# Performance work log

Measured on AMD Instinct MI355X. Metric: run time of the kernel, lower is better.

## Reference

```python
import jax, jax.numpy as jnp
import numpy as np

B, L, S, V = 1024, 512, 64, 160000
EMB = 16
E = 3 * EMB            # extended embedding dim = 48
G, M = 4, 3            # lsh_group_num, lsh_group_length
MAXC = 2 ** M          # 8 buckets per group
NH, KD = 8, 4          # MHA heads / key_dim
IN_DIM = 5 * EMB + 3 * E   # user(80) + item(48) + longterm(48) + shortterm(48) = 224
PAD_LT, PAD_ST = L // 4, S // 4
M_VALUES = jnp.array([1, 2, 4], dtype=jnp.float32)
LN_EPS = 1e-3  # keras LayerNormalization default


def setup_inputs() -> dict:
    key = jax.random.key(0)
    ks = list(jax.random.split(key, 40))
    d = {}
    for i, n in enumerate(['uid', 'utag1', 'utag2', 'utag3', 'utag4']):
        d[n] = jax.random.randint(ks[i], (B,), 1, V, dtype=jnp.int32)
    for i, n in enumerate(['label_goods_ids', 'label_shop_ids', 'label_cate_ids']):
        d[n] = jax.random.randint(ks[5 + i], (B,), 1, V, dtype=jnp.int32)
    for i, n in enumerate(['longterm_goods_ids', 'longterm_shop_ids', 'longterm_cate_ids']):
        ids = jax.random.randint(ks[8 + i], (B, L), 1, V, dtype=jnp.int32)
        d[n] = ids.at[:, L - PAD_LT:].set(0)  # left-aligned valid prefix, padded tail
    for i, n in enumerate(['shortterm_goods_ids', 'shortterm_shop_ids', 'shortterm_cate_ids']):
        ids = jax.random.randint(ks[11 + i], (B, S), 1, V, dtype=jnp.int32)
        d[n] = ids.at[:, S - PAD_ST:].set(0)
    def nrm(k, shape, s):
        return jax.random.normal(k, shape, jnp.float32) * s
    d['embed_table'] = nrm(ks[14], (V, EMB), 0.05)
    d['H'] = nrm(ks[15], (E, G, M), 1.0)  # non-trainable LSH projections
    d['wq'] = nrm(ks[16], (E, NH, KD), 0.1); d['bq'] = jnp.zeros((NH, KD))
    d['wk'] = nrm(ks[17], (E, NH, KD), 0.1); d['bk'] = jnp.zeros((NH, KD))
    d['wv'] = nrm(ks[18], (E, NH, KD), 0.1); d['bv'] = jnp.zeros((NH, KD))
    d['wo'] = nrm(ks[19], (NH, KD, E), 0.1); d['bo'] = jnp.zeros((E,))
    d['w1'] = nrm(ks[20], (IN_DIM, 200), 0.1); d['b1'] = jnp.zeros((200,))
    d['g1'] = jnp.ones((200,)); d['be1'] = jnp.zeros((200,))
    d['w2'] = nrm(ks[21], (200, 80), 0.1); d['b2'] = jnp.zeros((80,))
    d['g2'] = jnp.ones((80,)); d['be2'] = jnp.zeros((80,))
    d['w3'] = nrm(ks[22], (80, 1), 0.1); d['b3'] = jnp.zeros((1,))
    return d


def _stack_embed(table, feats):
    # feats: list of (B,) or (B,T) int arrays -> (B, T, n_feats*EMB)
    cols = [f[:, None] if f.ndim == 1 else f for f in feats]
    X = jnp.stack(cols, axis=2)              # (B, T, F)
    Xe = table[X]                            # (B, T, F, EMB)
    return Xe.reshape(Xe.shape[0], Xe.shape[1], -1)


def _layernorm(x, g, b):
    mu = x.mean(-1, keepdims=True)
    var = jnp.square(x - mu).mean(-1, keepdims=True)
    return g * (x - mu) / jnp.sqrt(var + LN_EPS) + b


def _lsh_codes(x, H):
    # x: (B, T, E) -> integer bucket codes (B, T, G)
    codes = jnp.sign(jnp.einsum('bte,egm->btgm', x, H))
    binary = (codes == 1).astype(jnp.float32)
    return jnp.tensordot(binary, M_VALUES, axes=[[-1], [0]]).astype(jnp.int32)


def _forward(uid, utag1, utag2, utag3, utag4,
             label_goods_ids, label_shop_ids, label_cate_ids,
             longterm_goods_ids, longterm_shop_ids, longterm_cate_ids,
             shortterm_goods_ids, shortterm_shop_ids, shortterm_cate_ids,
             embed_table, H, wq, bq, wk, bk, wv, bv, wo, bo,
             w1, b1, g1, be1, w2, b2, g2, be2, w3, b3):
    # --- embeddings ---
    Xu = _stack_embed(embed_table, [uid, utag1, utag2, utag3, utag4])        # (B,1,80)
    Xi = _stack_embed(embed_table, [label_goods_ids, label_shop_ids, label_cate_ids])  # (B,1,48)
    Xl = _stack_embed(embed_table, [longterm_goods_ids, longterm_shop_ids, longterm_cate_ids])   # (B,L,48)
    Xs = _stack_embed(embed_table, [shortterm_goods_ids, shortterm_shop_ids, shortterm_cate_ids])  # (B,S,48)

    longterm_pad = longterm_goods_ids == 0
    shortterm_pad = shortterm_goods_ids == 0

    # --- long-term interest: LSH scatter-mean over buckets then gather by item code ---
    series_int = _lsh_codes(Xl, H)                                   # (B,L,G)
    mXl = Xl * (~longterm_pad).astype(jnp.float32)[:, :, None]        # masked series embeddings
    oh = jax.nn.one_hot(series_int, MAXC, dtype=jnp.float32)          # (B,L,G,C)
    c_sum = jnp.einsum('blgc,ble->bgce', oh, mXl)                     # bucket sums (B,G,C,E)
    vc = oh.sum(axis=1)                                               # valid counts (B,G,C)
    safe = jnp.where(vc[..., None] > 0,
                     c_sum / jnp.maximum(vc[..., None], 1.0),
                     0.0)                                             # bucket means
    item_int = _lsh_codes(Xi, H)                                      # (B,1,G)
    item_oh = jax.nn.one_hot(item_int, MAXC, dtype=jnp.float32)       # (B,1,G,C)
    longterm_interest = jnp.einsum('bgce,bsgc->bsge', safe, item_oh).mean(axis=2)  # (B,1,E)

    # --- short-term interest: target attention (keras MultiHeadAttention) ---
    lengths = (~shortterm_pad).astype(jnp.int32).sum(axis=1)           # (B,)
    seq_mask = (jnp.arange(S)[None, :] < lengths[:, None]).astype(jnp.float32)  # (B,S)
    q = jnp.einsum('bqe,ehd->bqhd', Xi, wq) + bq
    k = jnp.einsum('bke,ehd->bkhd', Xs, wk) + bk
    v = jnp.einsum('bke,ehd->bkhd', Xs, wv) + bv
    scores = jnp.einsum('bqhd,bkhd->bhqk', q, k) / jnp.sqrt(jnp.float32(KD))
    scores = scores + (1.0 - seq_mask[:, None, None, :]) * (-1e9)
    attn = jax.nn.softmax(scores, axis=-1)
    ctx = jnp.einsum('bhqk,bkhd->bqhd', attn, v)
    shortterm_interest = jnp.einsum('bqhd,hde->bqe', ctx, wo) + bo      # (B,1,E)

    # --- final MLP: Dense->LN->ReLU x2, Dense->sigmoid ---
    feat = jnp.concatenate([Xu[:, 0], Xi[:, 0],
                            longterm_interest[:, 0], shortterm_interest[:, 0]], axis=-1)  # (B,224)
    h = jax.nn.relu(_layernorm(feat @ w1 + b1, g1, be1))
    h = jax.nn.relu(_layernorm(h @ w2 + b2, g2, be2))
    return jax.nn.sigmoid(h @ w3 + b3)                                 # (B,1)


def reference(uid, utag1, utag2, utag3, utag4,
              label_goods_ids, label_shop_ids, label_cate_ids,
              longterm_goods_ids, longterm_shop_ids, longterm_cate_ids,
              shortterm_goods_ids, shortterm_shop_ids, shortterm_cate_ids,
              embed_table, H, wq, bq, wk, bk, wv, bv, wo, bo,
              w1, b1, g1, be1, w2, b2, g2, be2, w3, b3):
    return _forward(uid, utag1, utag2, utag3, utag4,
                    label_goods_ids, label_shop_ids, label_cate_ids,
                    longterm_goods_ids, longterm_shop_ids, longterm_cate_ids,
                    shortterm_goods_ids, shortterm_shop_ids, shortterm_cate_ids,
                    embed_table, H, wq, bq, wk, bk, wv, bv, wo, bo,
                    w1, b1, g1, be1, w2, b2, g2, be2, w3, b3)
```

## Files before the change

kernel.cpp:

```cpp
#include <hip/hip_runtime.h>
#include <hip/hip_bf16.h>

#define LLEN 512
#define SLEN 64
#define EMBD 16
#define EE 48
#define GG 4
#define NHH 8
#define KDD 4
#define INDIM 224
#define H1D 200
#define H2D 80
#define CHUNK 128
#define PXE 52

__device__ __forceinline__ float bf2f(unsigned short u) {
    union { unsigned int i; float f; } v; v.i = ((unsigned int)u) << 16; return v.f;
}

template<bool BF16>
__device__ __forceinline__ float ldf(const void* p, int i) {
    if constexpr (BF16) return bf2f(((const unsigned short*)p)[i]);
    else                return ((const float*)p)[i];
}

template<bool BF16>
__device__ __forceinline__ float4 ld4(const void* p, int i4) {
    if constexpr (BF16) {
        ushort4 u = ((const ushort4*)p)[i4 >> 2];
        return make_float4(bf2f(u.x), bf2f(u.y), bf2f(u.z), bf2f(u.w));
    } else {
        return ((const float4*)p)[i4 >> 2];
    }
}

struct Pool {
    float buf[CHUNK * PXE + 16];
    float part[GG][GG][EE];
    float hf[12 * EE];
    float feat[INDIM];
    float q[NHH * KDD];
    float red[128];
    int   pc[2][GG];
    int   icode[GG];
    int   len;
    float mu, rstd;
};

template<bool BF16>
__device__ void sdim_body(Pool& P,
    const int* uid, const int* ut1, const int* ut2, const int* ut3, const int* ut4,
    const int* lb_g, const int* lb_s, const int* lb_c,
    const int* lt_g, const int* lt_s, const int* lt_c,
    const int* st_g, const int* st_s, const int* st_c,
    const void* tbl, const void* Hm,
    const void* wq, const void* bq, const void* wk, const void* bk,
    const void* wvv, const void* bv, const void* wo, const void* bo,
    const void* w1, const void* b1, const void* g1, const void* be1,
    const void* w2, const void* b2, const void* g2, const void* be2,
    const void* w3, const void* b3, void* outp)
{
    const int b = blockIdx.x;
    const int tid = threadIdx.x;
    const int lane = tid & 63;
    const int wid = __builtin_amdgcn_readfirstlane(tid >> 6);

    for (int i = tid; i < 12 * EE; i += 256) {
        int j = i / EE, e = i - j * EE;
        P.hf[i] = ldf<BF16>(Hm, e * 12 + j);
    }
    if (tid < 80) {
        int f = tid >> 4, e = tid & 15;
        int id = (f == 0) ? uid[b] : (f == 1) ? ut1[b] : (f == 2) ? ut2[b] : (f == 3) ? ut3[b] : ut4[b];
        P.feat[tid] = ldf<BF16>(tbl, id * EMBD + e);
    } else if (tid < 128) {
        int t = tid - 80; int f = t >> 4, e = t & 15;
        int id = (f == 0) ? lb_g[b] : (f == 1) ? lb_s[b] : lb_c[b];
        P.feat[80 + t] = ldf<BF16>(tbl, id * EMBD + e);
    }
    __syncthreads();

    if (tid < 32) {
        float acc = ldf<BF16>(bq, tid);
        for (int e = 0; e < EE; e++) acc += P.feat[80 + e] * ldf<BF16>(wq, e * 32 + tid);
        P.q[tid] = acc;
    }
    if (tid >= 64 && tid < 76) {
        int j = tid - 64;
        float acc = 0.f;
        for (int e = 0; e < EE; e++) acc += P.feat[80 + e] * P.hf[j * EE + e];
        P.red[j] = acc;
    }
    __syncthreads();
    if (tid < GG) {
        int code = 0;
        #pragma unroll
        for (int m = 0; m < 3; m++) if (P.red[tid * 3 + m] > 0.f) code |= (1 << m);
        P.icode[tid] = code;
    }

    float accg[GG] = {0.f, 0.f, 0.f, 0.f};
    int   cnt[GG]  = {0, 0, 0, 0};
    const int offs = (lane < 52) ? lane : 51;

    for (int ch = 0; ch < LLEN / CHUNK; ch++) {
        const int base = ch * CHUNK;
        {
            int ids[6];
            #pragma unroll
            for (int i = 0; i < 6; i++) {
                int f = tid + 256 * i;
                int p = f / 12, qq = f - 12 * p, fe = qq >> 2;
                const int* idp = (fe == 0) ? lt_g : (fe == 1) ? lt_s : lt_c;
                ids[i] = idp[b * LLEN + base + p];
            }
            float4 vs[6];
            #pragma unroll
            for (int i = 0; i < 6; i++) {
                int f = tid + 256 * i;
                int p = f / 12, qq = f - 12 * p;
                vs[i] = ld4<BF16>(tbl, ids[i] * EMBD + ((qq & 3) << 2));
            }
            #pragma unroll
            for (int i = 0; i < 6; i++) {
                int f = tid + 256 * i;
                int p = f / 12, qq = f - 12 * p;
                *(float4*)&P.buf[p * PXE + (qq << 2)] = vs[i];
            }
        }
        __syncthreads();
        if (!(wid & 1)) {
            const int p = ((wid >> 1) << 6) | lane;
            const float* row = &P.buf[p * PXE];
            float4 x[12];
            #pragma unroll
            for (int k = 0; k < 12; k++) x[k] = *(const float4*)(row + 4 * k);
            float acc[12];
            #pragma unroll
            for (int j = 0; j < 12; j++) {
                const float4* hr = (const float4*)&P.hf[j * EE];
                float s = 0.f;
                #pragma unroll
                for (int k = 0; k < 12; k++) {
                    float4 h4 = hr[k];
                    s += x[k].x * h4.x + x[k].y * h4.y + x[k].z * h4.z + x[k].w * h4.w;
                }
                acc[j] = s;
            }
            int code[GG];
            #pragma unroll
            for (int g = 0; g < GG; g++) {
                int c = 0;
                #pragma unroll
                for (int m = 0; m < 3; m++) if (acc[g * 3 + m] > 0.f) c |= (1 << m);
                code[g] = c;
            }
            int valid = (lt_g[b * LLEN + base + p] != 0);
            float4 sel;
            sel.x = (code[0] == P.icode[0] && valid) ? 1.f : 0.f;
            sel.y = (code[1] == P.icode[1] && valid) ? 1.f : 0.f;
            sel.z = (code[2] == P.icode[2] && valid) ? 1.f : 0.f;
            sel.w = (code[3] == P.icode[3] && valid) ? 1.f : 0.f;
            *(float4*)&P.buf[p * PXE + 48] = sel;
            #pragma unroll
            for (int g = 0; g < GG; g++)
                cnt[g] += __popcll(__ballot(code[g] == P.icode[g]));
        }
        __syncthreads();
        {
            const float* basep = &P.buf[(wid * 32) * PXE] + offs;
            #pragma unroll
            for (int i = 0; i < 32; i++) {
                float xv = basep[i * PXE];
                #pragma unroll
                for (int g = 0; g < GG; g++) {
                    float sel = __int_as_float(
                        __builtin_amdgcn_readlane(__float_as_int(xv), 48 + g));
                    accg[g] += sel * xv;
                }
            }
        }
        __syncthreads();
    }
    if (lane < EE) {
        #pragma unroll
        for (int g = 0; g < GG; g++) P.part[wid][g][lane] = accg[g];
    }
    if (!(wid & 1) && lane == 0) {
        #pragma unroll
        for (int g = 0; g < GG; g++) P.pc[wid >> 1][g] = cnt[g];
    }
    __syncthreads();

    if (tid < EE) {
        float r = 0.f;
        #pragma unroll
        for (int g = 0; g < GG; g++) {
            float c = (float)(P.pc[0][g] + P.pc[1][g]);
            float s = P.part[0][g][tid] + P.part[1][g][tid] + P.part[2][g][tid] + P.part[3][g][tid];
            r += s / fmaxf(c, 1.0f);
        }
        P.feat[128 + tid] = r * 0.25f;
    }

    float* Xs   = P.buf;
    float* wkq  = P.buf + SLEN * PXE;
    float* bkq  = wkq + EE * NHH;
    float* sc   = bkq + NHH;
    float* su   = sc + NHH * SLEN;
    float* sctx = su + NHH * EE;

    {
        int ids[3];
        #pragma unroll
        for (int i = 0; i < 3; i++) {
            int f = tid + 256 * i;
            int p = f / 12, qq = f - 12 * p, fe = qq >> 2;
            const int* idp = (fe == 0) ? st_g : (fe == 1) ? st_s : st_c;
            ids[i] = idp[b * SLEN + p];
        }
        float4 vs[3];
        #pragma unroll
        for (int i = 0; i < 3; i++) {
            int f = tid + 256 * i;
            int p = f / 12, qq = f - 12 * p;
            vs[i] = ld4<BF16>(tbl, ids[i] * EMBD + ((qq & 3) << 2));
        }
        #pragma unroll
        for (int i = 0; i < 3; i++) {
            int f = tid + 256 * i;
            int p = f / 12, qq = f - 12 * p;
            *(float4*)&Xs[p * PXE + (qq << 2)] = vs[i];
        }
    }
    if (tid < 64) {
        unsigned long long msk = __ballot(st_g[b * SLEN + tid] != 0);
        if (tid == 0) P.len = __popcll(msk);
    }
    for (int t = tid; t < EE * NHH; t += 256) {
        int e = t >> 3, h = t & 7;
        float acc = 0.f;
        #pragma unroll
        for (int d = 0; d < KDD; d++) acc += ldf<BF16>(wk, e * 32 + h * 4 + d) * P.q[h * 4 + d];
        wkq[t] = acc;
    }
    if (tid < NHH) {
        float acc = 0.f;
        #pragma unroll
        for (int d = 0; d < KDD; d++) acc += ldf<BF16>(bk, tid * 4 + d) * P.q[tid * 4 + d];
        bkq[tid] = acc;
    }
    __syncthreads();
    for (int t = tid; t < NHH * SLEN; t += 256) {
        int h = t >> 6, s = t & 63;
        float acc = bkq[h];
        for (int e = 0; e < EE; e++) acc += Xs[s * PXE + e] * wkq[e * NHH + h];
        acc *= 0.5f;
        if (s >= P.len) acc -= 1e9f;
        sc[h * SLEN + s] = acc;
    }
    __syncthreads();
    for (int h = wid; h < NHH; h += 4) {
        float v = sc[h * SLEN + lane];
        float mx = v;
        #pragma unroll
        for (int o = 32; o; o >>= 1) mx = fmaxf(mx, __shfl_xor(mx, o));
        float ex = __expf(v - mx);
        float sm = ex;
        #pragma unroll
        for (int o = 32; o; o >>= 1) sm += __shfl_xor(sm, o);
        sc[h * SLEN + lane] = ex / sm;
    }
    __syncthreads();
    for (int t = tid; t < NHH * EE; t += 256) {
        int h = t / EE, e = t - h * EE;
        float acc = 0.f;
        for (int s = 0; s < SLEN; s++) acc += sc[h * SLEN + s] * Xs[s * PXE + e];
        su[t] = acc;
    }
    __syncthreads();
    if (tid < 32) {
        float acc = ldf<BF16>(bv, tid);
        int h = tid >> 2;
        for (int e = 0; e < EE; e++) acc += su[h * EE + e] * ldf<BF16>(wvv, e * 32 + tid);
        sctx[tid] = acc;
    }
    __syncthreads();
    if (tid < EE) {
        float acc = ldf<BF16>(bo, tid);
        #pragma unroll
        for (int i = 0; i < 32; i++) acc += sctx[i] * ldf<BF16>(wo, i * EE + tid);
        P.feat[176 + tid] = acc;
    }
    __syncthreads();

    float z1 = 0.f;
    if (tid < H1D) {
        z1 = ldf<BF16>(b1, tid);
        for (int i = 0; i < INDIM; i++) z1 += P.feat[i] * ldf<BF16>(w1, i * H1D + tid);
        P.buf[tid] = z1;
    }
    __syncthreads();
    if (tid < 64) {
        float sm = 0.f, sq = 0.f;
        for (int j = tid; j < H1D; j += 64) { float v = P.buf[j]; sm += v; sq += v * v; }
        #pragma unroll
        for (int o = 32; o; o >>= 1) { sm += __shfl_xor(sm, o); sq += __shfl_xor(sq, o); }
        if (tid == 0) { float mu = sm / H1D; P.mu = mu; P.rstd = rsqrtf(sq / H1D - mu * mu + 1e-3f); }
    }
    __syncthreads();
    if (tid < H1D) {
        float h = fmaxf(ldf<BF16>(g1, tid) * (z1 - P.mu) * P.rstd + ldf<BF16>(be1, tid), 0.f);
        P.buf[256 + tid] = h;
    }
    __syncthreads();
    float z2 = 0.f;
    if (tid < H2D) {
        z2 = ldf<BF16>(b2, tid);
        for (int i = 0; i < H1D; i++) z2 += P.buf[256 + i] * ldf<BF16>(w2, i * H2D + tid);
        P.buf[tid] = z2;
    }
    __syncthreads();
    if (tid < 64) {
        float sm = 0.f, sq = 0.f;
        for (int j = tid; j < H2D; j += 64) { float v = P.buf[j]; sm += v; sq += v * v; }
        #pragma unroll
        for (int o = 32; o; o >>= 1) { sm += __shfl_xor(sm, o); sq += __shfl_xor(sq, o); }
        if (tid == 0) { float mu = sm / H2D; P.mu = mu; P.rstd = rsqrtf(sq / H2D - mu * mu + 1e-3f); }
    }
    __syncthreads();
    if (tid < H2D) {
        float h = fmaxf(ldf<BF16>(g2, tid) * (z2 - P.mu) * P.rstd + ldf<BF16>(be2, tid), 0.f);
        P.red[tid] = h * ldf<BF16>(w3, tid);
    }
    __syncthreads();
    if (tid == 0) {
        float acc = ldf<BF16>(b3, 0);
        for (int i = 0; i < H2D; i++) acc += P.red[i];
        float sig = 1.f / (1.f + __expf(-acc));
        if constexpr (BF16) ((__hip_bfloat16*)outp)[b] = __float2bfloat16(sig);
        else                ((float*)outp)[b] = sig;
    }
}

__global__ __launch_bounds__(256, 4) void sdim_fwd(
    const int* __restrict__ uid, const int* __restrict__ ut1, const int* __restrict__ ut2,
    const int* __restrict__ ut3, const int* __restrict__ ut4,
    const int* __restrict__ lb_g, const int* __restrict__ lb_s, const int* __restrict__ lb_c,
    const int* __restrict__ lt_g, const int* __restrict__ lt_s, const int* __restrict__ lt_c,
    const int* __restrict__ st_g, const int* __restrict__ st_s, const int* __restrict__ st_c,
    const void* __restrict__ tbl, const void* __restrict__ Hm,
    const void* __restrict__ wq, const void* __restrict__ bq,
    const void* __restrict__ wk, const void* __restrict__ bk,
    const void* __restrict__ wvv, const void* __restrict__ bv,
    const void* __restrict__ wo, const void* __restrict__ bo,
    const void* __restrict__ w1, const void* __restrict__ b1,
    const void* __restrict__ g1, const void* __restrict__ be1,
    const void* __restrict__ w2, const void* __restrict__ b2,
    const void* __restrict__ g2, const void* __restrict__ be2,
    const void* __restrict__ w3, const void* __restrict__ b3,
    void* __restrict__ outp)
{
    __shared__ Pool P;
    __shared__ int s_isbf;
    if (threadIdx.x < 64) {
        int big = 0;
        for (int i = (threadIdx.x & 63); i < 128; i += 64) {
            unsigned short u = ((const unsigned short*)tbl)[2 * i];
            if (((u >> 7) & 0xFF) >= 127) big = 1;
        }
        unsigned long long m = __ballot(big);
        if (threadIdx.x == 0) s_isbf = (m == 0ull) ? 1 : 0;
    }
    __syncthreads();
    if (s_isbf)
        sdim_body<true >(P, uid, ut1, ut2, ut3, ut4, lb_g, lb_s, lb_c, lt_g, lt_s, lt_c,
                         st_g, st_s, st_c, tbl, Hm, wq, bq, wk, bk, wvv, bv, wo, bo,
                         w1, b1, g1, be1, w2, b2, g2, be2, w3, b3, outp);
    else
        sdim_body<false>(P, uid, ut1, ut2, ut3, ut4, lb_g, lb_s, lb_c, lt_g, lt_s, lt_c,
                         st_g, st_s, st_c, tbl, Hm, wq, bq, wk, bk, wvv, bv, wo, bo,
                         w1, b1, g1, be1, w2, b2, g2, be2, w3, b3, outp);
}

extern "C" void kernel_launch(void* const* d_in, const int* in_sizes, int n_in,
                              void* d_out, int out_size, void* d_ws, size_t ws_size,
                              hipStream_t stream) {
    const int B = in_sizes[0];
    sdim_fwd<<<B, 256, 0, stream>>>(
        (const int*)d_in[0],  (const int*)d_in[1],  (const int*)d_in[2],
        (const int*)d_in[3],  (const int*)d_in[4],
        (const int*)d_in[5],  (const int*)d_in[6],  (const int*)d_in[7],
        (const int*)d_in[8],  (const int*)d_in[9],  (const int*)d_in[10],
        (const int*)d_in[11], (const int*)d_in[12], (const int*)d_in[13],
        (const void*)d_in[14], (const void*)d_in[15],
        (const void*)d_in[16], (const void*)d_in[17],
        (const void*)d_in[18], (const void*)d_in[19],
        (const void*)d_in[20], (const void*)d_in[21],
        (const void*)d_in[22], (const void*)d_in[23],
        (const void*)d_in[24], (const void*)d_in[25],
        (const void*)d_in[26], (const void*)d_in[27],
        (const void*)d_in[28], (const void*)d_in[29],
        (const void*)d_in[30], (const void*)d_in[31],
        (const void*)d_in[32], (const void*)d_in[33],
        d_out);
}
```

Baseline: 205.9 us.

## Move LSH projection matrix to global workspace and transpose short-term tile in LDS

Adds a tiny prep kernel that converts the LSH projection matrix H to fp32 in workspace, so each block reads it from global/cache with uniform (scalar-friendly) addresses instead of staging it in shared memory. The LSH projection loop is reordered to stream x per float4 and accumulate twelve outputs. The short-term embedding tile is stored transposed with a padded stride to reduce LDS bank conflicts in the attention score and context loops. This adds an extra launch and relies on the compiler hoisting uniform H loads; a null workspace falls back to reading H directly on every access.

```diff
diff --git a/kernel.cpp b/kernel.cpp
--- a/kernel.cpp
+++ b/kernel.cpp
@@ -13,6 +13,7 @@
 #define H2D 80
 #define CHUNK 128
 #define PXE 52
+#define TXS 65
 
 __device__ __forceinline__ float bf2f(unsigned short u) {
     union { unsigned int i; float f; } v; v.i = ((unsigned int)u) << 16; return v.f;
@@ -34,10 +35,28 @@
     }
 }
 
+template<bool BF16>
+__device__ __forceinline__ float ldh(const float* hf, const void* Hm, int i) {
+    return hf ? hf[i] : ldf<BF16>(Hm, i);
+}
+
+__global__ void prep_kernel(const unsigned short* __restrict__ tbl,
+                            const void* __restrict__ Hm, float* __restrict__ hf) {
+    int t = threadIdx.x;
+    int big = 0;
+    for (int i = t; i < 128; i += 64) {
+        unsigned short u = tbl[2 * i];
+        if (((u >> 7) & 0xFF) >= 127) big = 1;
+    }
+    unsigned long long m = __ballot(big);
+    int isbf = (m == 0ull) ? 1 : 0;
+    for (int i = t; i < EE * 12; i += 64)
+        hf[i] = isbf ? bf2f(((const unsigned short*)Hm)[i]) : ((const float*)Hm)[i];
+}
+
 struct Pool {
     float buf[CHUNK * PXE + 16];
     float part[GG][GG][EE];
-    float hf[12 * EE];
     float feat[INDIM];
     float q[NHH * KDD];
     float red[128];
@@ -58,17 +77,13 @@
     const void* wvv, const void* bv, const void* wo, const void* bo,
     const void* w1, const void* b1, const void* g1, const void* be1,
     const void* w2, const void* b2, const void* g2, const void* be2,
-    const void* w3, const void* b3, void* outp)
+    const void* w3, const void* b3, void* outp, const float* hf)
 {
     const int b = blockIdx.x;
     const int tid = threadIdx.x;
     const int lane = tid & 63;
     const int wid = __builtin_amdgcn_readfirstlane(tid >> 6);
 
-    for (int i = tid; i < 12 * EE; i += 256) {
-        int j = i / EE, e = i - j * EE;
-        P.hf[i] = ldf<BF16>(Hm, e * 12 + j);
-    }
     if (tid < 80) {
         int f = tid >> 4, e = tid & 15;
         int id = (f == 0) ? uid[b] : (f == 1) ? ut1[b] : (f == 2) ? ut2[b] : (f == 3) ? ut3[b] : ut4[b];
@@ -88,7 +103,7 @@
     if (tid >= 64 && tid < 76) {
         int j = tid - 64;
         float acc = 0.f;
-        for (int e = 0; e < EE; e++) acc += P.feat[80 + e] * P.hf[j * EE + e];
+        for (int e = 0; e < EE; e++) acc += P.feat[80 + e] * ldh<BF16>(hf, Hm, e * 12 + j);
         P.red[j] = acc;
     }
     __syncthreads();
@@ -132,20 +147,19 @@
         if (!(wid & 1)) {
             const int p = ((wid >> 1) << 6) | lane;
             const float* row = &P.buf[p * PXE];
-            float4 x[12];
-            #pragma unroll
-            for (int k = 0; k < 12; k++) x[k] = *(const float4*)(row + 4 * k);
             float acc[12];
             #pragma unroll
-            for (int j = 0; j < 12; j++) {
-                const float4* hr = (const float4*)&P.hf[j * EE];
-                float s = 0.f;
+            for (int j = 0; j < 12; j++) acc[j] = 0.f;
+            #pragma unroll
+            for (int k = 0; k < 12; k++) {
+                float4 x4 = *(const float4*)(row + 4 * k);
                 #pragma unroll
-                for (int k = 0; k < 12; k++) {
-                    float4 h4 = hr[k];
-                    s += x[k].x * h4.x + x[k].y * h4.y + x[k].z * h4.z + x[k].w * h4.w;
+                for (int j = 0; j < 12; j++) {
+                    acc[j] += x4.x * ldh<BF16>(hf, Hm, (4 * k + 0) * 12 + j)
+                            + x4.y * ldh<BF16>(hf, Hm, (4 * k + 1) * 12 + j)
+                            + x4.z * ldh<BF16>(hf, Hm, (4 * k + 2) * 12 + j)
+                            + x4.w * ldh<BF16>(hf, Hm, (4 * k + 3) * 12 + j);
                 }
-                acc[j] = s;
             }
             int code[GG];
             #pragma unroll
@@ -203,8 +217,8 @@
         P.feat[128 + tid] = r * 0.25f;
     }
 
-    float* Xs   = P.buf;
-    float* wkq  = P.buf + SLEN * PXE;
+    float* XsT  = P.buf;
+    float* wkq  = P.buf + EE * TXS;
     float* bkq  = wkq + EE * NHH;
     float* sc   = bkq + NHH;
     float* su   = sc + NHH * SLEN;
@@ -230,7 +244,10 @@
         for (int i = 0; i < 3; i++) {
             int f = tid + 256 * i;
             int p = f / 12, qq = f - 12 * p;
-            *(float4*)&Xs[p * PXE + (qq << 2)] = vs[i];
+            XsT[(4 * qq + 0) * TXS + p] = vs[i].x;
+            XsT[(4 * qq + 1) * TXS + p] = vs[i].y;
+            XsT[(4 * qq + 2) * TXS + p] = vs[i].z;
+            XsT[(4 * qq + 3) * TXS + p] = vs[i].w;
         }
     }
     if (tid < 64) {
@@ -254,7 +271,7 @@
     for (int t = tid; t < NHH * SLEN; t += 256) {
         int h = t >> 6, s = t & 63;
         float acc = bkq[h];
-        for (int e = 0; e < EE; e++) acc += Xs[s * PXE + e] * wkq[e * NHH + h];
+        for (int e = 0; e < EE; e++) acc += XsT[e * TXS + s] * wkq[e * NHH + h];
         acc *= 0.5f;
         if (s >= P.len) acc -= 1e9f;
         sc[h * SLEN + s] = acc;
@@ -275,7 +292,7 @@
     for (int t = tid; t < NHH * EE; t += 256) {
         int h = t / EE, e = t - h * EE;
         float acc = 0.f;
-        for (int s = 0; s < SLEN; s++) acc += sc[h * SLEN + s] * Xs[s * PXE + e];
+        for (int s = 0; s < SLEN; s++) acc += sc[h * SLEN + s] * XsT[e * TXS + s];
         su[t] = acc;
     }
     __syncthreads();
@@ -359,7 +376,7 @@
     const void* __restrict__ w2, const void* __restrict__ b2,
     const void* __restrict__ g2, const void* __restrict__ be2,
     const void* __restrict__ w3, const void* __restrict__ b3,
-    void* __restrict__ outp)
+    void* __restrict__ outp, const float* __restrict__ hf)
 {
     __shared__ Pool P;
     __shared__ int s_isbf;
@@ -376,17 +393,22 @@
     if (s_isbf)
         sdim_body<true >(P, uid, ut1, ut2, ut3, ut4, lb_g, lb_s, lb_c, lt_g, lt_s, lt_c,
                          st_g, st_s, st_c, tbl, Hm, wq, bq, wk, bk, wvv, bv, wo, bo,
-                         w1, b1, g1, be1, w2, b2, g2, be2, w3, b3, outp);
+                         w1, b1, g1, be1, w2, b2, g2, be2, w3, b3, outp, hf);
     else
         sdim_body<false>(P, uid, ut1, ut2, ut3, ut4, lb_g, lb_s, lb_c, lt_g, lt_s, lt_c,
                          st_g, st_s, st_c, tbl, Hm, wq, bq, wk, bk, wvv, bv, wo, bo,
-                         w1, b1, g1, be1, w2, b2, g2, be2, w3, b3, outp);
+                         w1, b1, g1, be1, w2, b2, g2, be2, w3, b3, outp, hf);
 }
 
 extern "C" void kernel_launch(void* const* d_in, const int* in_sizes, int n_in,
                               void* d_out, int out_size, void* d_ws, size_t ws_size,
                               hipStream_t stream) {
     const int B = in_sizes[0];
+    float* hf = nullptr;
+    if (ws_size >= (16 + EE * 12) * sizeof(float)) {
+        hf = (float*)d_ws + 16;
+        prep_kernel<<<1, 64, 0, stream>>>((const unsigned short*)d_in[14], d_in[15], hf);
+    }
     sdim_fwd<<<B, 256, 0, stream>>>(
         (const int*)d_in[0],  (const int*)d_in[1],  (const int*)d_in[2],
         (const int*)d_in[3],  (const int*)d_in[4],
@@ -403,5 +425,5 @@
         (const void*)d_in[28], (const void*)d_in[29],
         (const void*)d_in[30], (const void*)d_in[31],
         (const void*)d_in[32], (const void*)d_in[33],
-        d_out);
-}
+        d_out, hf);
+}
```

New measurement: 234.7 us. 1.14x slower.
